# Kernel optimization log

Measured on AMD Instinct MI355X. Metric: run time of the kernel, lower is better.

## Reference

```python
import jax, jax.numpy as jnp
import numpy as np

K = 3       # kernel_size
SIGMA = 0.1 # noise scale


def setup_inputs() -> dict:
    key = jax.random.key(0)
    k1, k2 = jax.random.split(key)
    img = jax.random.uniform(k1, (32, 3, 512, 512), dtype=jnp.float32)
    noise = jax.random.normal(k2, (32, K, K), dtype=jnp.float32)
    return {"img": img, "noise": noise}


def reference(img, noise):
    b, c, h, w = img.shape
    # delta impulse: note original uses center = ceil(k/2) -> index 2 for k=3
    center = int(np.ceil(K / 2))
    delta = jnp.zeros((K, K), dtype=img.dtype).at[center, center].set(1.0)
    weight = (SIGMA * noise + delta)[:, None, :, :]  # [b, 1, K, K]
    x = jnp.transpose(img, (1, 0, 2, 3))  # [c, b, h, w]: conv batch=c, channels=b
    y = jax.lax.conv_general_dilated(
        x, weight,
        window_strides=(1, 1), padding='SAME',
        dimension_numbers=('NCHW', 'OIHW', 'NCHW'),
        feature_group_count=b,
    )  # [c, b, h, w]
    y = jnp.where(jnp.isnan(y), jnp.asarray(1.0, y.dtype), y)
    y = jnp.transpose(y, (1, 0, 2, 3))  # back to [b, c, h, w]
    return jnp.clip(y, 0.0, 1.0)
```

## Files before the change

kernel.cpp:

```cpp
#include <hip/hip_runtime.h>


#define RF_H 512
#define RF_W 512
#define RF_C 3
#define RF_SIGMA 0.1f

typedef float floatx4 __attribute__((ext_vector_type(4)));

__global__ __launch_bounds__(256) void RandomFilter_40767829574170_kernel(
    const float* __restrict__ img,
    const float* __restrict__ noise,
    float* __restrict__ out)
{
    const int idx   = blockIdx.x * 256 + threadIdx.x;
    const int wg    = idx & 63;
    const int strip = (idx >> 6) & 127;
    const int plane = idx >> 13;
    const int b     = plane / RF_C;

    const float* P  = img + plane * (RF_H * RF_W);
    const int    w0 = wg * 8;
    const int    h0 = strip * 4;

    const int   offA = (wg > 0)  ? (w0 - 4) : w0;
    const int   offD = (wg < 63) ? (w0 + 8) : w0;
    const float mA   = (wg > 0)  ? 1.0f : 0.0f;
    const float mD   = (wg < 63) ? 1.0f : 0.0f;

    floatx4 R[6][4];
    #pragma unroll
    for (int r = 0; r < 6; ++r) {
        const int hr  = h0 - 1 + r;
        const int hrc = hr < 0 ? 0 : (hr > RF_H - 1 ? RF_H - 1 : hr);
        const float* row = P + (hrc << 9);
        R[r][0] = *reinterpret_cast<const floatx4*>(row + offA);
        R[r][1] = *reinterpret_cast<const floatx4*>(row + w0);
        R[r][2] = *reinterpret_cast<const floatx4*>(row + w0 + 4);
        R[r][3] = *reinterpret_cast<const floatx4*>(row + offD);
    }

    const float* np_ = noise + b * 9;
    float wgt[3][3];
    #pragma unroll
    for (int r = 0; r < 3; ++r)
        #pragma unroll
        for (int s = 0; s < 3; ++s)
            wgt[r][s] = RF_SIGMA * np_[r * 3 + s];
    wgt[2][2] += 1.0f;

    float acc[4][8];
    #pragma unroll
    for (int o = 0; o < 4; ++o)
        #pragma unroll
        for (int j = 0; j < 8; ++j) acc[o][j] = 0.0f;

    #pragma unroll
    for (int r = 0; r < 6; ++r) {
        float w_[10];
        w_[0] = R[r][0].w * mA;
        w_[1] = R[r][1].x; w_[2] = R[r][1].y; w_[3] = R[r][1].z; w_[4] = R[r][1].w;
        w_[5] = R[r][2].x; w_[6] = R[r][2].y; w_[7] = R[r][2].z; w_[8] = R[r][2].w;
        w_[9] = R[r][3].x * mD;
        if (r == 0 && h0 == 0) {
            #pragma unroll
            for (int k = 0; k < 10; ++k) w_[k] = 0.0f;
        }
        if (r == 5 && h0 == RF_H - 4) {
            #pragma unroll
            for (int k = 0; k < 10; ++k) w_[k] = 0.0f;
        }
        #pragma unroll
        for (int o = 0; o < 4; ++o) {
            const int kr = r - o;
            if (kr >= 0 && kr <= 2) {
                const float k0 = wgt[kr][0], k1 = wgt[kr][1], k2 = wgt[kr][2];
                #pragma unroll
                for (int j = 0; j < 8; ++j)
                    acc[o][j] += k0 * w_[j] + k1 * w_[j + 1] + k2 * w_[j + 2];
            }
        }
    }

    float* outP = out + plane * (RF_H * RF_W) + w0;
    #pragma unroll
    for (int o = 0; o < 4; ++o) {
        floatx4 lo, hi;
        lo.x = fminf(fmaxf(acc[o][0], 0.0f), 1.0f);
        lo.y = fminf(fmaxf(acc[o][1], 0.0f), 1.0f);
        lo.z = fminf(fmaxf(acc[o][2], 0.0f), 1.0f);
        lo.w = fminf(fmaxf(acc[o][3], 0.0f), 1.0f);
        hi.x = fminf(fmaxf(acc[o][4], 0.0f), 1.0f);
        hi.y = fminf(fmaxf(acc[o][5], 0.0f), 1.0f);
        hi.z = fminf(fmaxf(acc[o][6], 0.0f), 1.0f);
        hi.w = fminf(fmaxf(acc[o][7], 0.0f), 1.0f);
        float* orow = outP + ((h0 + o) << 9);
        *reinterpret_cast<floatx4*>(orow)     = lo;
        *reinterpret_cast<floatx4*>(orow + 4) = hi;
    }
}

extern "C" void kernel_launch(void* const* d_in, const int* in_sizes, int n_in,
                              void* d_out, int out_size, void* d_ws, size_t ws_size,
                              hipStream_t stream) {
    const float* img   = (const float*)d_in[0];
    const float* noise = (const float*)d_in[1];
    float* out = (float*)d_out;

    const int grid = 96 * 128 * 64 / 256;
    RandomFilter_40767829574170_kernel<<<grid, 256, 0, stream>>>(img, noise, out);
}
```

Measured before the change: 41.42 us.

## Replace halo loads with wavefront shuffles and swizzle block-to-plane mapping

```diff
diff --git a/kernel.cpp b/kernel.cpp
--- a/kernel.cpp
+++ b/kernel.cpp
@@ -3,7 +3,6 @@
 
 #define RF_H 512
 #define RF_W 512
-#define RF_C 3
 #define RF_SIGMA 0.1f
 
 typedef float floatx4 __attribute__((ext_vector_type(4)));
@@ -13,32 +12,21 @@
     const float* __restrict__ noise,
     float* __restrict__ out)
 {
-    const int idx   = blockIdx.x * 256 + threadIdx.x;
-    const int wg    = idx & 63;
+    const int orig = blockIdx.x;
+    const int bid  = (orig & 7) * 384 + (orig >> 3);
+
+    const int idx   = bid * 256 + threadIdx.x;
+    const int lane  = idx & 63;
     const int strip = (idx >> 6) & 127;
     const int plane = idx >> 13;
-    const int b     = plane / RF_C;
+    const int b     = plane / 3;
 
     const float* P  = img + plane * (RF_H * RF_W);
-    const int    w0 = wg * 8;
-    const int    h0 = strip * 4;
+    const int    w0 = lane << 3;
+    const int    h0 = strip << 2;
 
-    const int   offA = (wg > 0)  ? (w0 - 4) : w0;
-    const int   offD = (wg < 63) ? (w0 + 8) : w0;
-    const float mA   = (wg > 0)  ? 1.0f : 0.0f;
-    const float mD   = (wg < 63) ? 1.0f : 0.0f;
-
-    floatx4 R[6][4];
-    #pragma unroll
-    for (int r = 0; r < 6; ++r) {
-        const int hr  = h0 - 1 + r;
-        const int hrc = hr < 0 ? 0 : (hr > RF_H - 1 ? RF_H - 1 : hr);
-        const float* row = P + (hrc << 9);
-        R[r][0] = *reinterpret_cast<const floatx4*>(row + offA);
-        R[r][1] = *reinterpret_cast<const floatx4*>(row + w0);
-        R[r][2] = *reinterpret_cast<const floatx4*>(row + w0 + 4);
-        R[r][3] = *reinterpret_cast<const floatx4*>(row + offD);
-    }
+    const float mA = (lane > 0)  ? 1.0f : 0.0f;
+    const float mD = (lane < 63) ? 1.0f : 0.0f;
 
     const float* np_ = noise + b * 9;
     float wgt[3][3];
@@ -57,19 +45,21 @@
 
     #pragma unroll
     for (int r = 0; r < 6; ++r) {
+        const int hr  = h0 - 1 + r;
+        const int hrc = hr < 0 ? 0 : (hr > RF_H - 1 ? RF_H - 1 : hr);
+        const float* row = P + (hrc << 9);
+        const floatx4 Bv = *reinterpret_cast<const floatx4*>(row + w0);
+        const floatx4 Cv = *reinterpret_cast<const floatx4*>(row + w0 + 4);
+        const float left  = __shfl_up(Cv.w, 1);
+        const float right = __shfl_down(Bv.x, 1);
+        const float zf = (hr < 0 || hr >= RF_H) ? 0.0f : 1.0f;
+
         float w_[10];
-        w_[0] = R[r][0].w * mA;
-        w_[1] = R[r][1].x; w_[2] = R[r][1].y; w_[3] = R[r][1].z; w_[4] = R[r][1].w;
-        w_[5] = R[r][2].x; w_[6] = R[r][2].y; w_[7] = R[r][2].z; w_[8] = R[r][2].w;
-        w_[9] = R[r][3].x * mD;
-        if (r == 0 && h0 == 0) {
-            #pragma unroll
-            for (int k = 0; k < 10; ++k) w_[k] = 0.0f;
-        }
-        if (r == 5 && h0 == RF_H - 4) {
-            #pragma unroll
-            for (int k = 0; k < 10; ++k) w_[k] = 0.0f;
-        }
+        w_[0] = left * mA * zf;
+        w_[1] = Bv.x * zf; w_[2] = Bv.y * zf; w_[3] = Bv.z * zf; w_[4] = Bv.w * zf;
+        w_[5] = Cv.x * zf; w_[6] = Cv.y * zf; w_[7] = Cv.z * zf; w_[8] = Cv.w * zf;
+        w_[9] = right * mD * zf;
+
         #pragma unroll
         for (int o = 0; o < 4; ++o) {
             const int kr = r - o;
```

Measured after the change: 36.17 us, median of 2. 1.15x faster.
